# Performance work log

Measured on AMD Instinct MI355X. Metric: run time of the kernel, lower is better.

The kernel has to match this reference:

```python
import jax, jax.numpy as jnp
import numpy as np

QLEN, MLEN, BSZ, D_MODEL, N_HEAD, D_HEAD = 1024, 1024, 4, 1024, 16, 64
KLEN = QLEN + MLEN
LN_EPS = 1e-5


def _linear(x, W, b):
    return x @ W + b


def _layer_norm(x, g, b):
    mu = jnp.mean(x, axis=-1, keepdims=True)
    var = jnp.var(x, axis=-1, keepdims=True)
    return (x - mu) * jax.lax.rsqrt(var + LN_EPS) * g + b


def _rel_shift(x):
    # x: [b, n, q, k] -> Transformer-XL rel-shift via zero-pad + reshape trick
    b, n, q, k = x.shape
    x = jnp.pad(x, ((0, 0), (0, 0), (0, 0), (1, 0)))
    x = x.reshape(b, n, k + 1, q)[:, :, 1:, :].reshape(b, n, q, k)
    return x


def setup_inputs() -> dict:
    key = jax.random.key(0)
    ks = jax.random.split(key, 16)
    s = 0.02
    inp = {
        "w": jax.random.normal(ks[0], (QLEN, BSZ, D_MODEL), jnp.float32),
        "r": jax.random.normal(ks[1], (KLEN, D_MODEL), jnp.float32),
        "r_w_bias": jax.random.normal(ks[2], (N_HEAD, D_HEAD), jnp.float32) * s,
        "r_r_bias": jax.random.normal(ks[3], (N_HEAD, D_HEAD), jnp.float32) * s,
        "mems": jax.random.normal(ks[4], (MLEN, BSZ, D_MODEL), jnp.float32),
        "Wq": jax.random.normal(ks[5], (D_MODEL, N_HEAD * D_HEAD), jnp.float32) * s,
        "bq": jnp.zeros((N_HEAD * D_HEAD,), jnp.float32),
        "Wk": jax.random.normal(ks[6], (D_MODEL, N_HEAD * D_HEAD), jnp.float32) * s,
        "bk": jnp.zeros((N_HEAD * D_HEAD,), jnp.float32),
        "Wv": jax.random.normal(ks[7], (D_MODEL, N_HEAD * D_HEAD), jnp.float32) * s,
        "bv": jnp.zeros((N_HEAD * D_HEAD,), jnp.float32),
        "Wr": jax.random.normal(ks[8], (D_MODEL, N_HEAD * D_HEAD), jnp.float32) * s,
        "br": jnp.zeros((N_HEAD * D_HEAD,), jnp.float32),
        "Wo": jax.random.normal(ks[9], (N_HEAD * D_HEAD, D_MODEL), jnp.float32) * s,
        "bo": jnp.zeros((D_MODEL,), jnp.float32),
        "ln_g": jnp.ones((D_MODEL,), jnp.float32),
        "ln_b": jnp.zeros((D_MODEL,), jnp.float32),
    }
    # causal mask with memory: key j visible to query i iff j <= i + MLEN
    inp["attn_mask"] = jnp.arange(KLEN)[None, :] > (jnp.arange(QLEN)[:, None] + MLEN)
    return inp


def reference(w, r, r_w_bias, r_r_bias, mems, Wq, bq, Wk, bk, Wv, bv, Wr, br,
              Wo, bo, ln_g, ln_b, attn_mask):
    qlen, bsz = w.shape[0], w.shape[1]
    scale = 1.0 / (D_HEAD ** 0.5)

    cat = jnp.concatenate([mems, w], axis=0)               # [klen, b, d]
    klen = cat.shape[0]

    q = _linear(cat, Wq, bq)[-qlen:]                       # [q, b, n*d]
    k = _linear(cat, Wk, bk)                               # [k, b, n*d]
    v = _linear(cat, Wv, bv)
    rk = _linear(r, Wr, br)                                # [rlen, n*d]

    q = q.reshape(qlen, bsz, N_HEAD, D_HEAD)
    k = k.reshape(klen, bsz, N_HEAD, D_HEAD)
    v = v.reshape(klen, bsz, N_HEAD, D_HEAD)
    rk = rk.reshape(r.shape[0], N_HEAD, D_HEAD)

    AC = jnp.einsum('ibnd,jbnd->bnij', q + r_w_bias, k)
    BD = jnp.einsum('ibnd,jnd->bnij', q + r_r_bias, rk)
    BD = _rel_shift(BD)

    attn_score = scale * (AC + BD)                          # [b, n, q, k]
    attn_score = jnp.where(attn_mask[None, None, :, :], -jnp.inf, attn_score)
    attn_prob = jax.nn.softmax(attn_score, axis=3)

    attn_vec = jnp.einsum('bnij,jbnd->ibnd', attn_prob, v)
    attn_vec = attn_vec.reshape(qlen, bsz, N_HEAD * D_HEAD)
    attn_out = _linear(attn_vec, Wo, bo)

    return _layer_norm(w + attn_out, ln_g, ln_b)            # post-lnorm path
```

## Files before the change

kernel.cpp:

```cpp
#include <hip/hip_runtime.h>
#include <stdint.h>


typedef unsigned short u16;
typedef unsigned int u32;
typedef __attribute__((ext_vector_type(8))) short s16x8;
typedef __attribute__((ext_vector_type(4))) float f32x4;

typedef const __attribute__((address_space(1))) void gvoid;
typedef __attribute__((address_space(3))) void lvoid;

__device__ __forceinline__ void async16(const u16* g, u16* l) {
  __builtin_amdgcn_global_load_lds((gvoid*)g, (lvoid*)l, 16, 0, 0);
}

__device__ __forceinline__ float b2f(u16 h) {
  union { u32 u; float f; } v; v.u = ((u32)h) << 16; return v.f;
}
__device__ __forceinline__ u16 f2b(float f) {
  union { float f; u32 u; } v; v.f = f; u32 u = v.u;
  return (u16)((u + 0x7FFFu + ((u >> 16) & 1u)) >> 16);
}
__device__ __forceinline__ bool is_bf16(const u16* lng) { return lng[0] == 0x3F80u; }

__device__ __forceinline__ void ld8(const void* p, size_t idx, bool bf, u16* dst) {
  if (bf) {
    *(uint4*)dst = *(const uint4*)((const u16*)p + idx);
  } else {
    const float* f = (const float*)p + idx;
    float4 a = *(const float4*)f;
    float4 c = *(const float4*)(f + 4);
    dst[0] = f2b(a.x); dst[1] = f2b(a.y); dst[2] = f2b(a.z); dst[3] = f2b(a.w);
    dst[4] = f2b(c.x); dst[5] = f2b(c.y); dst[6] = f2b(c.z); dst[7] = f2b(c.w);
  }
}
__device__ __forceinline__ float ldS(const void* p, int idx, bool bf) {
  return bf ? b2f(((const u16*)p)[idx]) : ((const float*)p)[idx];
}

__device__ __forceinline__ void gemm_bt_body(
    u16* As, u16* Bs,
    const void* Alo, const void* Ahi, int splitRow,
    const u16* BT, const void* bias,
    const void* eb0, const void* eb1,
    u16* C0, u16* C1, bool bfin, bool abf,
    int bm, int bnc)
{
  const int t = threadIdx.x;
  const int lane = t & 63, w = t >> 6;
  const int wr = w >> 1, wc = w & 1;
  const int ml = lane & 15, q = lane >> 4;

  f32x4 zero4 = {0.f, 0.f, 0.f, 0.f};
  f32x4 acc[4][4];
#pragma unroll
  for (int i = 0; i < 4; ++i)
#pragma unroll
    for (int j = 0; j < 4; ++j) acc[i][j] = zero4;

  const int srow = t >> 2;
  const int sch  = t & 3;
  const void* aptr[2]; size_t aidx[2]; const u16* bsrc[2];
#pragma unroll
  for (int p = 0; p < 2; ++p) {
    int gr = bm + srow + p * 64;
    if (gr < splitRow) { aptr[p] = Alo; aidx[p] = (size_t)gr * 1024 + sch * 8; }
    else { aptr[p] = Ahi; aidx[p] = (size_t)(gr - splitRow) * 1024 + sch * 8; }
    bsrc[p] = BT + (size_t)(bnc + srow + p * 64) * 1024 + sch * 8;
  }
  u16* lA[2] = { As + t * 8, As + 2048 + t * 8 };
  u16* lB[2] = { Bs + t * 8, Bs + 2048 + t * 8 };

  for (int kk = 0; kk < 1024; kk += 32) {
    if (abf) {
      __syncthreads();
      async16((const u16*)aptr[0] + aidx[0] + kk, lA[0]);
      async16((const u16*)aptr[1] + aidx[1] + kk, lA[1]);
      async16(bsrc[0] + kk, lB[0]);
      async16(bsrc[1] + kk, lB[1]);
      __syncthreads();
    } else {
      u16 ta0[8], ta1[8];
      ld8(aptr[0], aidx[0] + kk, false, ta0);
      ld8(aptr[1], aidx[1] + kk, false, ta1);
      uint4 vb0 = *(const uint4*)(bsrc[0] + kk);
      uint4 vb1 = *(const uint4*)(bsrc[1] + kk);
      __syncthreads();
      *(uint4*)lA[0] = *(uint4*)ta0;
      *(uint4*)lA[1] = *(uint4*)ta1;
      *(uint4*)lB[0] = vb0;
      *(uint4*)lB[1] = vb1;
      __syncthreads();
    }
    s16x8 af[4], bf[4];
#pragma unroll
    for (int mi = 0; mi < 4; ++mi)
      af[mi] = *(const s16x8*)&As[(wr * 64 + mi * 16 + ml) * 32 + q * 8];
#pragma unroll
    for (int ni = 0; ni < 4; ++ni)
      bf[ni] = *(const s16x8*)&Bs[(wc * 64 + ni * 16 + ml) * 32 + q * 8];
#pragma unroll
    for (int mi = 0; mi < 4; ++mi)
#pragma unroll
      for (int ni = 0; ni < 4; ++ni)
        acc[mi][ni] = __builtin_amdgcn_mfma_f32_16x16x32_bf16(af[mi], bf[ni],
                                                              acc[mi][ni], 0, 0, 0);
  }

#pragma unroll
  for (int ni = 0; ni < 4; ++ni) {
    int gcol = bnc + wc * 64 + ni * 16 + ml;
    float bi = ldS(bias, gcol, bfin);
    float e0 = eb0 ? ldS(eb0, gcol, bfin) : 0.f;
    float e1 = eb1 ? ldS(eb1, gcol, bfin) : 0.f;
#pragma unroll
    for (int mi = 0; mi < 4; ++mi)
#pragma unroll
      for (int rr = 0; rr < 4; ++rr) {
        int grow = bm + wr * 64 + mi * 16 + 4 * q + rr;
        size_t off = (size_t)grow * 1024 + gcol;
        float v0 = acc[mi][ni][rr] + bi;
        if (C1) { C0[off] = f2b(v0 + e0); C1[off] = f2b(v0 + e1); }
        else    { C0[off] = f2b(v0); }
      }
  }
}

__device__ __forceinline__ void gemm_vt_body(
    u16* As, u16* Bs,
    const void* Mlo, const void* Whi,
    const u16* WvT, const void* bv,
    u16* vT, bool bfin,
    int j0, int nc0, int b)
{
  const int t = threadIdx.x;
  const int lane = t & 63, w = t >> 6;
  const int wr = w >> 1, wc = w & 1;
  const int ml = lane & 15, q = lane >> 4;

  f32x4 zero4 = {0.f, 0.f, 0.f, 0.f};
  f32x4 acc[4][4];
#pragma unroll
  for (int i = 0; i < 4; ++i)
#pragma unroll
    for (int j = 0; j < 4; ++j) acc[i][j] = zero4;

  const int srow = t >> 2, sch = t & 3;
  const u16* asrc[2]; const void* bptr[2]; size_t bidx[2];
#pragma unroll
  for (int p = 0; p < 2; ++p) {
    asrc[p] = WvT + (size_t)(nc0 + srow + p * 64) * 1024 + sch * 8;
    int j = j0 + srow + p * 64;
    if (j < 1024) { bptr[p] = Mlo; bidx[p] = ((size_t)j * 4 + b) * 1024 + sch * 8; }
    else { bptr[p] = Whi; bidx[p] = ((size_t)(j - 1024) * 4 + b) * 1024 + sch * 8; }
  }
  u16* lA[2] = { As + t * 8, As + 2048 + t * 8 };
  u16* lB[2] = { Bs + t * 8, Bs + 2048 + t * 8 };

  for (int kk = 0; kk < 1024; kk += 32) {
    if (bfin) {
      __syncthreads();
      async16(asrc[0] + kk, lA[0]);
      async16(asrc[1] + kk, lA[1]);
      async16((const u16*)bptr[0] + bidx[0] + kk, lB[0]);
      async16((const u16*)bptr[1] + bidx[1] + kk, lB[1]);
      __syncthreads();
    } else {
      u16 tb0[8], tb1[8];
      ld8(bptr[0], bidx[0] + kk, false, tb0);
      ld8(bptr[1], bidx[1] + kk, false, tb1);
      __syncthreads();
      async16(asrc[0] + kk, lA[0]);
      async16(asrc[1] + kk, lA[1]);
      *(uint4*)lB[0] = *(uint4*)tb0;
      *(uint4*)lB[1] = *(uint4*)tb1;
      __syncthreads();
    }
    s16x8 af[4], bf[4];
#pragma unroll
    for (int mi = 0; mi < 4; ++mi)
      af[mi] = *(const s16x8*)&As[(wr * 64 + mi * 16 + ml) * 32 + q * 8];
#pragma unroll
    for (int ni = 0; ni < 4; ++ni)
      bf[ni] = *(const s16x8*)&Bs[(wc * 64 + ni * 16 + ml) * 32 + q * 8];
#pragma unroll
    for (int mi = 0; mi < 4; ++mi)
#pragma unroll
      for (int ni = 0; ni < 4; ++ni)
        acc[mi][ni] = __builtin_amdgcn_mfma_f32_16x16x32_bf16(af[mi], bf[ni],
                                                              acc[mi][ni], 0, 0, 0);
  }

#pragma unroll
  for (int mi = 0; mi < 4; ++mi)
#pragma unroll
    for (int rr = 0; rr < 4; ++rr) {
      int nc = nc0 + wr * 64 + mi * 16 + 4 * q + rr;
      float bi = ldS(bv, nc, bfin);
      size_t rbase = ((size_t)b * 1024 + nc) * 2048 + j0 + wc * 64 + ml * 4;
      u32 w0 = (u32)f2b(acc[mi][0][rr] + bi) | ((u32)f2b(acc[mi][1][rr] + bi) << 16);
      u32 w1 = (u32)f2b(acc[mi][2][rr] + bi) | ((u32)f2b(acc[mi][3][rr] + bi) << 16);
      uint2 pk; pk.x = w0; pk.y = w1;
      *(uint2*)(vT + rbase) = pk;
    }
}

__global__ __launch_bounds__(256) void gemm_bt(
    const void* __restrict__ Alo, const void* __restrict__ Ahi, int splitRow,
    const u16* __restrict__ BT, const void* __restrict__ bias,
    const void* __restrict__ eb0, const void* __restrict__ eb1,
    u16* __restrict__ C0, u16* __restrict__ C1,
    const u16* __restrict__ lng, int aIsInput)
{
  __shared__ u16 As[128 * 32];
  __shared__ u16 Bs[128 * 32];
  const bool bfin = is_bf16(lng);
  const bool abf = aIsInput ? bfin : true;
  int lin = blockIdx.y * gridDim.x + blockIdx.x;
  int nwg = gridDim.x * gridDim.y;
  int cpx = nwg >> 3;
  int id  = (lin & 7) * cpx + (lin >> 3);
  int bx = id % gridDim.x, by = id / gridDim.x;
  gemm_bt_body(As, Bs, Alo, Ahi, splitRow, BT, bias, eb0, eb1, C0, C1,
               bfin, abf, by * 128, bx * 128);
}

__global__ __launch_bounds__(256) void proj_uber(
    const void* __restrict__ mems, const void* __restrict__ w,
    const void* __restrict__ r,
    const u16* __restrict__ WkT, const void* __restrict__ bk,
    const u16* __restrict__ WvT, const void* __restrict__ bv,
    const u16* __restrict__ WqT, const void* __restrict__ bq,
    const void* __restrict__ rwb, const void* __restrict__ rrb,
    const u16* __restrict__ WrT, const void* __restrict__ br,
    u16* __restrict__ kb, u16* __restrict__ vT,
    u16* __restrict__ qw, u16* __restrict__ qr, u16* __restrict__ rkb,
    const u16* __restrict__ lng)
{
  __shared__ u16 As[128 * 32];
  __shared__ u16 Bs[128 * 32];
  const bool bfin = is_bf16(lng);
  int id = blockIdx.x;
  id = (id & 7) * 176 + (id >> 3);

  if (id < 512) {
    int bx = id & 7, by = id >> 3;
    gemm_bt_body(As, Bs, mems, w, 4096, WkT, bk, nullptr, nullptr,
                 kb, nullptr, bfin, bfin, by * 128, bx * 128);
  } else if (id < 1024) {
    int local = id - 512;
    int jx = local & 15, ny = (local >> 4) & 7, b = local >> 7;
    gemm_vt_body(As, Bs, mems, w, WvT, bv, vT, bfin, jx * 128, ny * 128, b);
  } else if (id < 1280) {
    int local = id - 1024;
    int bx = local & 7, by = local >> 3;
    gemm_bt_body(As, Bs, w, w, 4096, WqT, bq, rwb, rrb,
                 qw, qr, bfin, bfin, by * 128, bx * 128);
  } else {
    int local = id - 1280;
    int bx = local & 7, by = local >> 3;
    gemm_bt_body(As, Bs, r, r, 1 << 30, WrT, br, nullptr, nullptr,
                 rkb, nullptr, bfin, bfin, by * 128, bx * 128);
  }
}

__global__ __launch_bounds__(256) void transpose_w5(
    const void* __restrict__ W0, const void* __restrict__ W1,
    const void* __restrict__ W2, const void* __restrict__ W3,
    const void* __restrict__ W4,
    u16* __restrict__ T0, u16* __restrict__ T1, u16* __restrict__ T2,
    u16* __restrict__ T3, u16* __restrict__ T4, const u16* __restrict__ lng)
{
  __shared__ u16 tile[64 * 72];
  const bool bf = is_bf16(lng);
  const void* W; u16* T;
  switch (blockIdx.z) {
    case 0: W = W0; T = T0; break;
    case 1: W = W1; T = T1; break;
    case 2: W = W2; T = T2; break;
    case 3: W = W3; T = T3; break;
    default: W = W4; T = T4; break;
  }
  const int t = threadIdx.x;
  const int k0 = blockIdx.y * 64, n0 = blockIdx.x * 64;
#pragma unroll
  for (int p = 0; p < 2; ++p) {
    int s = p * 256 + t, row = s >> 3, ch = s & 7;
    u16 tmp[8];
    ld8(W, (size_t)(k0 + row) * 1024 + n0 + ch * 8, bf, tmp);
    *(uint4*)&tile[row * 72 + ch * 8] = *(uint4*)tmp;
  }
  __syncthreads();
#pragma unroll
  for (int p = 0; p < 2; ++p) {
    int s = p * 256 + t, nrow = s >> 3, ch = s & 7;
    union { u16 u[8]; uint4 v; } pk;
#pragma unroll
    for (int jj = 0; jj < 8; ++jj) pk.u[jj] = tile[(ch * 8 + jj) * 72 + nrow];
    *(uint4*)(T + (size_t)(n0 + nrow) * 1024 + k0 + ch * 8) = pk.v;
  }
}

__global__ __launch_bounds__(512, 4) void flash_attn(
    const u16* __restrict__ qw, const u16* __restrict__ qr,
    const u16* __restrict__ kb, const u16* __restrict__ vt,
    const u16* __restrict__ rkb, u16* __restrict__ av)
{
  constexpr int LP = 72;
  __shared__ u16 Ks[64 * LP];
  __shared__ u16 Vs[64 * LP];
  __shared__ u16 Rs[192 * LP];
  __shared__ u16 Ps[8][16 * LP];

  const int t = threadIdx.x;
  const int lane = t & 63, w = t >> 6;
  const int ml = lane & 15, q = lane >> 4;
  const int hbid = blockIdx.y * 8 + blockIdx.x;
  const int lbid = (hbid & 7) * 64 + (hbid >> 3);
  const int L = lbid & 63;
  const int i0idx = (L < 32) ? (L & 7) : 7 - (L & 7);
  const int i0 = i0idx * 128;
  const int bn = lbid >> 3, b = bn >> 4, nh = bn & 15;

  s16x8 aqw[2], aqr[2];
  {
    size_t qo = ((size_t)(i0 + 16 * w + ml) * 4 + b) * 1024 + nh * 64 + q * 8;
    aqw[0] = *(const s16x8*)(qw + qo);
    aqw[1] = *(const s16x8*)(qw + qo + 32);
    aqr[0] = *(const s16x8*)(qr + qo);
    aqr[1] = *(const s16x8*)(qr + qo + 32);
  }

  f32x4 zero4 = {0.f, 0.f, 0.f, 0.f};
  f32x4 o[4];
#pragma unroll
  for (int dt = 0; dt < 4; ++dt) o[dt] = zero4;
  float lsum[4] = {0.f, 0.f, 0.f, 0.f};

  const int ntiles = min(i0 / 64 + 18, 32);
  const int c_lo = 16 * (7 - w);
  const int srow = t >> 3, sch = t & 7;

  uint4 pK, pV, pR;
  auto issue_kv = [&](int jt) {
    const int j0n = jt * 64;
    pK = *(const uint4*)(kb + ((size_t)(j0n + srow) * 4 + b) * 1024 + nh * 64 + sch * 8);
    pV = *(const uint4*)(vt + ((size_t)bn * 64 + srow) * 2048 + j0n + sch * 8);
  };
  auto rload = [&](int g) {
    g = g < 0 ? 0 : (g > 2047 ? 2047 : g);
    return *(const uint4*)(rkb + (size_t)g * 1024 + nh * 64 + sch * 8);
  };

  {
    issue_kv(0);
    uint4 r0 = rload(896 - i0 + srow);
    uint4 r1 = rload(896 - i0 + srow + 64);
    uint4 r2 = rload(896 - i0 + srow + 128);
    *(uint4*)&Ks[srow * LP + sch * 8] = pK;
    *(uint4*)&Vs[srow * LP + sch * 8] = pV;
    *(uint4*)&Rs[(srow      ) * LP + sch * 8] = r0;
    *(uint4*)&Rs[(srow +  64) * LP + sch * 8] = r1;
    *(uint4*)&Rs[(srow + 128) * LP + sch * 8] = r2;
  }
  __syncthreads();

  int slab = 0;
  int rbase = c_lo;
  for (int jt = 0; jt < ntiles; ++jt) {
    const int j0 = jt * 64;
    if (jt > 0) {
      __syncthreads();
      *(uint4*)&Ks[srow * LP + sch * 8] = pK;
      *(uint4*)&Vs[srow * LP + sch * 8] = pV;
      *(uint4*)&Rs[(slab * 64 + srow) * LP + sch * 8] = pR;
      slab = slab == 2 ? 0 : slab + 1;
      rbase += 64; if (rbase >= 192) rbase -= 192;
      __syncthreads();
    }
    if (jt + 1 < ntiles) {
      issue_kv(jt + 1);
      pR = rload(64 * jt + 1088 - i0 + srow);
    }

    f32x4 sac[4];
#pragma unroll
    for (int tt = 0; tt < 4; ++tt) sac[tt] = zero4;
#pragma unroll
    for (int ki = 0; ki < 2; ++ki)
#pragma unroll
      for (int tt = 0; tt < 4; ++tt) {
        s16x8 bfr = *(const s16x8*)&Ks[(tt * 16 + ml) * LP + ki * 32 + q * 8];
        sac[tt] = __builtin_amdgcn_mfma_f32_16x16x32_bf16(aqw[ki], bfr, sac[tt], 0, 0, 0);
      }

    f32x4 g[5];
#pragma unroll
    for (int ct = 0; ct < 5; ++ct) g[ct] = zero4;
#pragma unroll
    for (int ct = 0; ct < 5; ++ct) {
      int pb = rbase + ct * 16; if (pb >= 192) pb -= 192;
      const u16* rp = &Rs[(pb + ml) * LP + q * 8];
      s16x8 b0 = *(const s16x8*)(rp);
      s16x8 b1 = *(const s16x8*)(rp + 32);
      g[ct] = __builtin_amdgcn_mfma_f32_16x16x32_bf16(aqr[0], b0, g[ct], 0, 0, 0);
      g[ct] = __builtin_amdgcn_mfma_f32_16x16x32_bf16(aqr[1], b1, g[ct], 0, 0, 0);
    }

    const bool mtile = (j0 + 63) > (i0 + 1024);

#pragma unroll
    for (int rr = 0; rr < 4; ++rr) {
      const int r = 4 * q + rr;
      const int irow = i0 + 16 * w + r;
      const int L2 = ((ml - r + 15) & 15) | (q << 4);
      const bool hs = ml < 15 - r;
      float bl0 = hs ? g[1][rr] : g[0][rr];
      float bl1 = hs ? g[2][rr] : g[1][rr];
      float bl2 = hs ? g[3][rr] : g[2][rr];
      float bl3 = hs ? g[4][rr] : g[3][rr];
      float band0 = __shfl(bl0, L2, 64);
      float band1 = __shfl(bl1, L2, 64);
      float band2 = __shfl(bl2, L2, 64);
      float band3 = __shfl(bl3, L2, 64);
      float s0 = 0.125f * (sac[0][rr] + band0);
      float s1 = 0.125f * (sac[1][rr] + band1);
      float s2 = 0.125f * (sac[2][rr] + band2);
      float s3 = 0.125f * (sac[3][rr] + band3);
      if (mtile) {
        int lim = irow + 1024 - j0 - ml;
        if (0 > lim)  s0 = -3.0e38f;
        if (16 > lim) s1 = -3.0e38f;
        if (32 > lim) s2 = -3.0e38f;
        if (48 > lim) s3 = -3.0e38f;
      }
      float p0 = __expf(s0), p1 = __expf(s1), p2 = __expf(s2), p3 = __expf(s3);
      lsum[rr] += (p0 + p1) + (p2 + p3);
      u32 w0 = (u32)f2b(p0) | ((u32)f2b(p1) << 16);
      u32 w1 = (u32)f2b(p2) | ((u32)f2b(p3) << 16);
      uint2 pk; pk.x = w0; pk.y = w1;
      *(uint2*)&Ps[w][r * LP + ml * 4] = pk;
    }

#pragma unroll
    for (int ki = 0; ki < 2; ++ki) {
      s16x8 a = *(const s16x8*)&Ps[w][ml * LP + ki * 32 + q * 8];
#pragma unroll
      for (int dt = 0; dt < 4; ++dt) {
        s16x8 bfr = *(const s16x8*)&Vs[(dt * 16 + ml) * LP + ki * 32 + q * 8];
        o[dt] = __builtin_amdgcn_mfma_f32_16x16x32_bf16(a, bfr, o[dt], 0, 0, 0);
      }
    }
  }

#pragma unroll
  for (int rr = 0; rr < 4; ++rr) {
    float l = lsum[rr];
#pragma unroll
    for (int off = 1; off < 16; off <<= 1) l += __shfl_xor(l, off);
    float inv = 1.f / l;
    int i = i0 + 16 * w + 4 * q + rr;
#pragma unroll
    for (int dt = 0; dt < 4; ++dt)
      av[((size_t)i * 4 + b) * 1024 + nh * 64 + dt * 16 + ml] = f2b(o[dt][rr] * inv);
  }
}

__global__ __launch_bounds__(256) void ln_kernel(
    const void* __restrict__ wi, const u16* __restrict__ ao,
    const void* __restrict__ gg, const void* __restrict__ bb,
    void* __restrict__ out)
{
  __shared__ float red[8];
  const bool bf = is_bf16((const u16*)gg);
  const int t = threadIdx.x;
  const int row = blockIdx.x;
  const int base = row * 1024 + t * 4;
  float x0, x1, x2, x3;
  if (bf) {
    ushort4 xw = *(const ushort4*)((const u16*)wi + base);
    x0 = b2f(xw.x); x1 = b2f(xw.y); x2 = b2f(xw.z); x3 = b2f(xw.w);
  } else {
    float4 xw = *(const float4*)((const float*)wi + base);
    x0 = xw.x; x1 = xw.y; x2 = xw.z; x3 = xw.w;
  }
  ushort4 xa = *(const ushort4*)(ao + base);
  x0 += b2f(xa.x); x1 += b2f(xa.y); x2 += b2f(xa.z); x3 += b2f(xa.w);
  float s = x0 + x1 + x2 + x3;
  float s2 = x0 * x0 + x1 * x1 + x2 * x2 + x3 * x3;
#pragma unroll
  for (int off = 1; off < 64; off <<= 1) {
    s += __shfl_xor(s, off);
    s2 += __shfl_xor(s2, off);
  }
  if ((t & 63) == 0) { red[t >> 6] = s; red[4 + (t >> 6)] = s2; }
  __syncthreads();
  float S = red[0] + red[1] + red[2] + red[3];
  float S2 = red[4] + red[5] + red[6] + red[7];
  float mu = S * (1.f / 1024.f);
  float var = S2 * (1.f / 1024.f) - mu * mu;
  float inv = rsqrtf(var + 1e-5f);
  float g0 = ldS(gg, t * 4 + 0, bf), g1 = ldS(gg, t * 4 + 1, bf);
  float g2 = ldS(gg, t * 4 + 2, bf), g3 = ldS(gg, t * 4 + 3, bf);
  float b0 = ldS(bb, t * 4 + 0, bf), b1 = ldS(bb, t * 4 + 1, bf);
  float b2v = ldS(bb, t * 4 + 2, bf), b3 = ldS(bb, t * 4 + 3, bf);
  float y0 = (x0 - mu) * inv * g0 + b0;
  float y1 = (x1 - mu) * inv * g1 + b1;
  float y2 = (x2 - mu) * inv * g2 + b2v;
  float y3 = (x3 - mu) * inv * g3 + b3;
  if (bf) {
    ushort4 r;
    r.x = f2b(y0); r.y = f2b(y1); r.z = f2b(y2); r.w = f2b(y3);
    *(ushort4*)((u16*)out + base) = r;
  } else {
    float4 r; r.x = y0; r.y = y1; r.z = y2; r.w = y3;
    *(float4*)((float*)out + base) = r;
  }
}

__global__ __launch_bounds__(256) void copy_w(
    const void* __restrict__ wi, const u16* __restrict__ lng,
    void* __restrict__ out)
{
  const bool bf = is_bf16(lng);
  int i = blockIdx.x * 256 + threadIdx.x;
  if (bf) ((u16*)out)[i] = ((const u16*)wi)[i];
  else    ((float*)out)[i] = ((const float*)wi)[i];
}

extern "C" void kernel_launch(void* const* d_in, const int* in_sizes, int n_in,
                              void* d_out, int out_size, void* d_ws, size_t ws_size,
                              hipStream_t stream) {
  (void)in_sizes; (void)n_in; (void)out_size;
  const void* w    = d_in[0];
  const void* r    = d_in[1];
  const void* rwb  = d_in[2];
  const void* rrb  = d_in[3];
  const void* mems = d_in[4];
  const void* Wq   = d_in[5];
  const void* bq   = d_in[6];
  const void* Wk   = d_in[7];
  const void* bk   = d_in[8];
  const void* Wv   = d_in[9];
  const void* bv   = d_in[10];
  const void* Wr   = d_in[11];
  const void* br   = d_in[12];
  const void* Wo   = d_in[13];
  const void* bo   = d_in[14];
  const u16*  lng  = (const u16*)d_in[15];
  const void* lnb  = d_in[16];

  dim3 blk(256);
  const size_t M = (size_t)1 << 20;
  const size_t NEED = 31 * M * 2;
  if (ws_size < NEED) {
    copy_w<<<dim3(16384), blk, 0, stream>>>(w, lng, d_out);
    return;
  }

  u16* ws  = (u16*)d_ws;
  u16* WqT = ws + 0 * M;
  u16* WkT = ws + 1 * M;
  u16* WvT = ws + 2 * M;
  u16* WrT = ws + 3 * M;
  u16* WoT = ws + 4 * M;
  u16* kb  = ws + 5 * M;
  u16* vT  = ws + 13 * M;
  u16* qw  = ws + 21 * M;
  u16* qr  = ws + 25 * M;
  u16* rkb = ws + 29 * M;
  u16* av  = ws + 0 * M;
  u16* ao  = qw;

  transpose_w5<<<dim3(16, 16, 5), blk, 0, stream>>>(Wq, Wk, Wv, Wr, Wo,
                                                    WqT, WkT, WvT, WrT, WoT, lng);
  proj_uber<<<dim3(1408), blk, 0, stream>>>(mems, w, r,
                                            WkT, bk, WvT, bv, WqT, bq, rwb, rrb,
                                            WrT, br, kb, vT, qw, qr, rkb, lng);
  flash_attn<<<dim3(8, 64), dim3(512), 0, stream>>>(qw, qr, kb, vT, rkb, av);
  gemm_bt<<<dim3(8, 32), blk, 0, stream>>>(av, av, 1 << 30, WoT, bo,
                                           nullptr, nullptr, ao, nullptr, lng, 0);
  ln_kernel<<<dim3(4096), blk, 0, stream>>>(w, ao, lng, lnb, d_out);
}
```

Baseline: 345.9 us.

## Store K and R head-major and load attention fragments directly from global

```diff
diff --git a/kernel.cpp b/kernel.cpp
--- a/kernel.cpp
+++ b/kernel.cpp
@@ -44,7 +44,7 @@
     const u16* BT, const void* bias,
     const void* eb0, const void* eb1,
     u16* C0, u16* C1, bool bfin, bool abf,
-    int bm, int bnc)
+    int bm, int bnc, int kmode)
 {
   const int t = threadIdx.x;
   const int lane = t & 63, w = t >> 6;
@@ -118,10 +118,20 @@
 #pragma unroll
       for (int rr = 0; rr < 4; ++rr) {
         int grow = bm + wr * 64 + mi * 16 + 4 * q + rr;
-        size_t off = (size_t)grow * 1024 + gcol;
         float v0 = acc[mi][ni][rr] + bi;
-        if (C1) { C0[off] = f2b(v0 + e0); C1[off] = f2b(v0 + e1); }
-        else    { C0[off] = f2b(v0); }
+        if (kmode == 1) {
+          size_t off = (((size_t)((grow & 3) * 16 + (gcol >> 6))) << 17)
+                     + ((size_t)(grow >> 2) << 6) + (gcol & 63);
+          C0[off] = f2b(v0);
+        } else if (kmode == 2) {
+          size_t off = (((size_t)(gcol >> 6)) << 17)
+                     + ((size_t)grow << 6) + (gcol & 63);
+          C0[off] = f2b(v0);
+        } else {
+          size_t off = (size_t)grow * 1024 + gcol;
+          if (C1) { C0[off] = f2b(v0 + e0); C1[off] = f2b(v0 + e1); }
+          else    { C0[off] = f2b(v0); }
+        }
       }
   }
 }
@@ -222,7 +232,7 @@
   int id  = (lin & 7) * cpx + (lin >> 3);
   int bx = id % gridDim.x, by = id / gridDim.x;
   gemm_bt_body(As, Bs, Alo, Ahi, splitRow, BT, bias, eb0, eb1, C0, C1,
-               bfin, abf, by * 128, bx * 128);
+               bfin, abf, by * 128, bx * 128, 0);
 }
 
 __global__ __launch_bounds__(256) void proj_uber(
@@ -246,7 +256,7 @@
   if (id < 512) {
     int bx = id & 7, by = id >> 3;
     gemm_bt_body(As, Bs, mems, w, 4096, WkT, bk, nullptr, nullptr,
-                 kb, nullptr, bfin, bfin, by * 128, bx * 128);
+                 kb, nullptr, bfin, bfin, by * 128, bx * 128, 1);
   } else if (id < 1024) {
     int local = id - 512;
     int jx = local & 15, ny = (local >> 4) & 7, b = local >> 7;
@@ -255,12 +265,12 @@
     int local = id - 1024;
     int bx = local & 7, by = local >> 3;
     gemm_bt_body(As, Bs, w, w, 4096, WqT, bq, rwb, rrb,
-                 qw, qr, bfin, bfin, by * 128, bx * 128);
+                 qw, qr, bfin, bfin, by * 128, bx * 128, 0);
   } else {
     int local = id - 1280;
     int bx = local & 7, by = local >> 3;
     gemm_bt_body(As, Bs, r, r, 1 << 30, WrT, br, nullptr, nullptr,
-                 rkb, nullptr, bfin, bfin, by * 128, bx * 128);
+                 rkb, nullptr, bfin, bfin, by * 128, bx * 128, 2);
   }
 }
 
@@ -307,9 +317,7 @@
     const u16* __restrict__ rkb, u16* __restrict__ av)
 {
   constexpr int LP = 72;
-  __shared__ u16 Ks[64 * LP];
   __shared__ u16 Vs[64 * LP];
-  __shared__ u16 Rs[192 * LP];
   __shared__ u16 Ps[8][16 * LP];
 
   const int t = threadIdx.x;
@@ -331,6 +339,10 @@
     aqr[1] = *(const s16x8*)(qr + qo + 32);
   }
 
+  const u16* kbase = kb  + ((size_t)bn << 17);
+  const u16* rbase = rkb + ((size_t)nh << 17);
+  const int fo = ml * 64 + q * 8;
+
   f32x4 zero4 = {0.f, 0.f, 0.f, 0.f};
   f32x4 o[4];
 #pragma unroll
@@ -341,47 +353,23 @@
   const int c_lo = 16 * (7 - w);
   const int srow = t >> 3, sch = t & 7;
 
-  uint4 pK, pV, pR;
-  auto issue_kv = [&](int jt) {
-    const int j0n = jt * 64;
-    pK = *(const uint4*)(kb + ((size_t)(j0n + srow) * 4 + b) * 1024 + nh * 64 + sch * 8);
-    pV = *(const uint4*)(vt + ((size_t)bn * 64 + srow) * 2048 + j0n + sch * 8);
+  uint4 pV;
+  auto vload = [&](int jt) {
+    return *(const uint4*)(vt + ((size_t)bn * 64 + srow) * 2048 + jt * 64 + sch * 8);
   };
-  auto rload = [&](int g) {
-    g = g < 0 ? 0 : (g > 2047 ? 2047 : g);
-    return *(const uint4*)(rkb + (size_t)g * 1024 + nh * 64 + sch * 8);
-  };
-
-  {
-    issue_kv(0);
-    uint4 r0 = rload(896 - i0 + srow);
-    uint4 r1 = rload(896 - i0 + srow + 64);
-    uint4 r2 = rload(896 - i0 + srow + 128);
-    *(uint4*)&Ks[srow * LP + sch * 8] = pK;
-    *(uint4*)&Vs[srow * LP + sch * 8] = pV;
-    *(uint4*)&Rs[(srow      ) * LP + sch * 8] = r0;
-    *(uint4*)&Rs[(srow +  64) * LP + sch * 8] = r1;
-    *(uint4*)&Rs[(srow + 128) * LP + sch * 8] = r2;
-  }
+
+  pV = vload(0);
+  *(uint4*)&Vs[srow * LP + sch * 8] = pV;
   __syncthreads();
 
-  int slab = 0;
-  int rbase = c_lo;
   for (int jt = 0; jt < ntiles; ++jt) {
     const int j0 = jt * 64;
     if (jt > 0) {
       __syncthreads();
-      *(uint4*)&Ks[srow * LP + sch * 8] = pK;
       *(uint4*)&Vs[srow * LP + sch * 8] = pV;
-      *(uint4*)&Rs[(slab * 64 + srow) * LP + sch * 8] = pR;
-      slab = slab == 2 ? 0 : slab + 1;
-      rbase += 64; if (rbase >= 192) rbase -= 192;
-      __syncthreads();
-    }
-    if (jt + 1 < ntiles) {
-      issue_kv(jt + 1);
-      pR = rload(64 * jt + 1088 - i0 + srow);
-    }
+      __syncthreads();
+    }
+    if (jt + 1 < ntiles) pV = vload(jt + 1);
 
     f32x4 sac[4];
 #pragma unroll
@@ -390,17 +378,19 @@
     for (int ki = 0; ki < 2; ++ki)
 #pragma unroll
       for (int tt = 0; tt < 4; ++tt) {
-        s16x8 bfr = *(const s16x8*)&Ks[(tt * 16 + ml) * LP + ki * 32 + q * 8];
-        sac[tt] = __builtin_amdgcn_mfma_f32_16x16x32_bf16(aqw[ki], bfr, sac[tt], 0, 0, 0);
+        s16x8 kf = *(const s16x8*)(kbase + (size_t)(j0 + tt * 16) * 64 + ki * 32 + fo);
+        sac[tt] = __builtin_amdgcn_mfma_f32_16x16x32_bf16(aqw[ki], kf, sac[tt], 0, 0, 0);
       }
 
+    const int jrb = j0 - i0 + 896 + c_lo;
     f32x4 g[5];
 #pragma unroll
     for (int ct = 0; ct < 5; ++ct) g[ct] = zero4;
 #pragma unroll
     for (int ct = 0; ct < 5; ++ct) {
-      int pb = rbase + ct * 16; if (pb >= 192) pb -= 192;
-      const u16* rp = &Rs[(pb + ml) * LP + q * 8];
+      int jr = jrb + ct * 16 + ml;
+      jr = jr < 0 ? 0 : (jr > 2047 ? 2047 : jr);
+      const u16* rp = rbase + ((size_t)jr << 6) + q * 8;
       s16x8 b0 = *(const s16x8*)(rp);
       s16x8 b1 = *(const s16x8*)(rp + 32);
       g[ct] = __builtin_amdgcn_mfma_f32_16x16x32_bf16(aqr[0], b0, g[ct], 0, 0, 0);
```

New measurement: 508.1 us. +46.9%, slower.
